# Kernel optimization log

Hardware: AMD Instinct MI355X
Metric: run time of the kernel (lower is better)

Reference implementation:

```python
import jax, jax.numpy as jnp
import numpy as np
from jax import lax

EPS = 1e-5
B, C, H, W = 16, 256, 56, 56
HEADS, DIM_K, DIM_U, DIM_OUT = 4, 16, 4, 256
DIM_V = DIM_OUT // HEADS  # 64
R = 15


def setup_inputs() -> dict:
    key = jax.random.key(0)
    ks = jax.random.split(key, 16)
    s = 0.05
    return {
        "x": jax.random.normal(ks[0], (B, C, H, W), jnp.float32),
        "Wq": jax.random.normal(ks[1], (C, HEADS * DIM_K), jnp.float32) * s,
        "Wk": jax.random.normal(ks[2], (C, DIM_U * DIM_K), jnp.float32) * s,
        "Wv": jax.random.normal(ks[3], (C, DIM_U * DIM_V), jnp.float32) * s,
        "pos_w": jax.random.normal(ks[4], (DIM_K, DIM_U, 1, R, R), jnp.float32) * s,
        "pos_b": jax.random.normal(ks[5], (DIM_K,), jnp.float32) * s,
        "gq": jax.random.uniform(ks[6], (HEADS * DIM_K,), jnp.float32),
        "bq": jax.random.normal(ks[7], (HEADS * DIM_K,), jnp.float32) * s,
        "mq": jax.random.normal(ks[8], (HEADS * DIM_K,), jnp.float32) * s,
        "vq": jax.random.uniform(ks[9], (HEADS * DIM_K,), jnp.float32) + 0.5,
        "gv": jax.random.uniform(ks[10], (DIM_U * DIM_V,), jnp.float32),
        "bv": jax.random.normal(ks[11], (DIM_U * DIM_V,), jnp.float32) * s,
        "mv": jax.random.normal(ks[12], (DIM_U * DIM_V,), jnp.float32) * s,
        "vv": jax.random.uniform(ks[13], (DIM_U * DIM_V,), jnp.float32) + 0.5,
    }


def _bn(x, gamma, beta, mean, var):
    # inference-mode BatchNorm over channel dim (axis=1), x: [b,c,h,w]
    inv = gamma / jnp.sqrt(var + EPS)
    return x * inv[None, :, None, None] + (beta - mean * inv)[None, :, None, None]


def reference(x, Wq, Wk, Wv, pos_w, pos_b, gq, bq, mq, vq, gv, bv, mv, vv):
    b, c, hh, ww = x.shape
    n = hh * ww
    h, dk, u, dv = HEADS, DIM_K, DIM_U, DIM_V
    # 1x1 convs (channels_first) == channel matmuls
    q = jnp.einsum('bchw,cd->bdhw', x, Wq)
    k = jnp.einsum('bchw,cd->bdhw', x, Wk)
    v = jnp.einsum('bchw,cd->bdhw', x, Wv)
    q = _bn(q, gq, bq, mq, vq)
    v = _bn(v, gv, bv, mv, vv)
    # rearranges: 'b (h k) hh ww -> b h k (hh ww)', 'b (u k) hh ww -> b u k n', 'b (u v) hh ww -> b u v n'
    q = q.reshape(b, h, dk, n)
    k = k.reshape(b, u, dk, n)
    v = v.reshape(b, u, dv, n)
    k = jax.nn.softmax(k, axis=-1)  # keras Softmax default axis=-1 (positions)
    # content lambda
    Lc = jnp.einsum('bukm,buvm->bkv', k, v)
    Yc = jnp.einsum('bhkn,bkv->bnhv', q, Lc)
    # position lambda: conv3d over (v,hh,ww) with kernel (1,r,r), pad spatial only
    v5 = v.reshape(b, u, dv, hh, ww)  # [N, C=u, D=v, H, W]
    p = R // 2
    Lp = lax.conv_general_dilated(
        v5, pos_w, window_strides=(1, 1, 1),
        padding=[(0, 0), (p, p), (p, p)],
        dimension_numbers=('NCDHW', 'OIDHW', 'NCDHW'))
    Lp = Lp + pos_b[None, :, None, None, None]  # [b, k, v, hh, ww]
    Lp = Lp.reshape(b, dk, dv, n)
    Yp = jnp.einsum('bhkn,bkvn->bnhv', q, Lp)
    Y = Yc + Yp  # [b, n, h, v]
    # 'b (hh ww) h v -> b (h v) hh ww'
    out = Y.reshape(b, hh, ww, h, dv).transpose(0, 3, 4, 1, 2).reshape(b, h * dv, hh, ww)
    return out
```

## Files before the change

kernel.cpp:

```cpp
#include <hip/hip_runtime.h>
#include <cstdint>
#include <cstddef>

#define NB   16
#define NC   256
#define NPIX 3136
#define NW   56
#define EPSV 1e-5f

#define OFF_AB   0u
#define OFF_BNA  49152u
#define OFF_BNB  49536u
#define OFF_WT   49920u
#define OFF_KS   58112u
#define OFF_LC   59136u
#define OFF_Y    75520u

typedef short bf16x8 __attribute__((ext_vector_type(8)));
typedef float f32x4  __attribute__((ext_vector_type(4)));
typedef float f32x16 __attribute__((ext_vector_type(16)));

__device__ __forceinline__ uint32_t f2bf(float f) {
  uint32_t x = __float_as_uint(f);
  uint32_t r = x + 0x7fffu + ((x >> 16) & 1u);
  return r >> 16;
}
__device__ __forceinline__ uint32_t pk_trunc(float a, float b) {
  return (__float_as_uint(a) >> 16) | (__float_as_uint(b) & 0xffff0000u);
}

__device__ __forceinline__ float fetchW(const float* Wq, const float* Wk,
                                        const float* Wv, int m, int c) {
  if (m < 64)  return Wq[c * 64 + m];
  if (m < 128) return Wk[c * 64 + (m - 64)];
  return Wv[c * 256 + (m - 128)];
}

__global__ void prep_kernel(const float* __restrict__ Wq, const float* __restrict__ Wk,
                            const float* __restrict__ Wv, const float* __restrict__ pos_w,
                            const float* __restrict__ gq, const float* __restrict__ bq,
                            const float* __restrict__ mq, const float* __restrict__ vq,
                            const float* __restrict__ gv, const float* __restrict__ bv,
                            const float* __restrict__ mv, const float* __restrict__ vv,
                            float* __restrict__ ws) {
  int d = blockIdx.x;
  int c = threadIdx.x;
  int i = d * 256 + c;
  if (i < 49152) {
    int dgt = i >> 12, rem = i & 4095;
    int kc = rem >> 8, rem2 = rem & 255;
    int lane = rem2 >> 2, dp = rem2 & 3;
    int m = dgt * 32 + (lane & 31);
    int k0 = kc * 16 + (lane >> 5) * 8 + dp * 2;
    float w0 = fetchW(Wq, Wk, Wv, m, k0);
    float w1 = fetchW(Wq, Wk, Wv, m, k0 + 1);
    ((uint32_t*)(ws + OFF_AB))[i] = f2bf(w0) | (f2bf(w1) << 16);
  }
  if (c == 0) {
    float sa, sb;
    if (d < 64)        { float inv = gq[d] / sqrtf(vq[d] + EPSV); sa = inv; sb = bq[d] - mq[d] * inv; }
    else if (d < 128)  { sa = 1.0f; sb = 0.0f; }
    else               { int j = d - 128; float inv = gv[j] / sqrtf(vv[j] + EPSV); sa = inv; sb = bv[j] - mv[j] * inv; }
    ws[OFF_BNA + d] = sa;
    ws[OFF_BNB + d] = sb;
  }
  if (i < 8192) {
    int chunk = i >> 8, rem = i & 255, lane = rem >> 2, dp = rem & 3;
    int quad = lane >> 4, k = lane & 15;
    int u = chunk >> 3, t = chunk & 7;
    int dh = 2 * t + (quad >> 1);
    int dwb = (quad & 1) * 8 + dp * 2;
    float w0 = (dh < 15 && dwb     < 15) ? pos_w[k * 900 + u * 225 + dh * 15 + dwb]     : 0.0f;
    float w1 = (dh < 15 && dwb + 1 < 15) ? pos_w[k * 900 + u * 225 + dh * 15 + dwb + 1] : 0.0f;
    ((uint32_t*)(ws + OFF_WT))[i] = f2bf(w0) | (f2bf(w1) << 16);
  }
  if (i < 1024) ws[OFF_KS + i] = 0.0f;
}

__launch_bounds__(256, 2)
__global__ void qkv_mfma(const float* __restrict__ x, const float* __restrict__ wsc,
                         float* __restrict__ Y) {
  __shared__ uint32_t X[64 * 128];
  __shared__ float BNs[768];
  int tid = threadIdx.x;
  int n0 = blockIdx.x * 64, b = blockIdx.y;
  for (int i = tid; i < 768; i += 256) BNs[i] = wsc[OFF_BNA + i];
  const size_t xb = (size_t)b * NC * NPIX;
#pragma unroll
  for (int it = 0; it < 4; ++it) {
    int n2 = tid & 31;
    int cp4 = it * 8 + (tid >> 5);
    const float* xp = x + xb + (size_t)(cp4 * 8) * NPIX + n0 + n2 * 2;
    float2 ld[8];
#pragma unroll
    for (int j = 0; j < 8; ++j) ld[j] = *(const float2*)(xp + (size_t)j * NPIX);
    uint32_t e0, e1, e2, e3, o0, o1, o2, o3;
    e0 = f2bf(ld[0].x) | (f2bf(ld[1].x) << 16);
    e1 = f2bf(ld[2].x) | (f2bf(ld[3].x) << 16);
    e2 = f2bf(ld[4].x) | (f2bf(ld[5].x) << 16);
    e3 = f2bf(ld[6].x) | (f2bf(ld[7].x) << 16);
    o0 = f2bf(ld[0].y) | (f2bf(ld[1].y) << 16);
    o1 = f2bf(ld[2].y) | (f2bf(ld[3].y) << 16);
    o2 = f2bf(ld[4].y) | (f2bf(ld[5].y) << 16);
    o3 = f2bf(ld[6].y) | (f2bf(ld[7].y) << 16);
    int ne = 2 * n2, no = ne + 1;
    uint4 ve; ve.x = e0; ve.y = e1; ve.z = e2; ve.w = e3;
    uint4 vo; vo.x = o0; vo.y = o1; vo.z = o2; vo.w = o3;
    *(uint4*)(X + ne * 128 + ((cp4 ^ (ne & 31)) << 2)) = ve;
    *(uint4*)(X + no * 128 + ((cp4 ^ (no & 31)) << 2)) = vo;
  }
  __syncthreads();
  int lane = tid & 63, w = tid >> 6;
  int n31 = lane & 31, h5 = lane >> 5;
  f32x16 acc[3][2];
#pragma unroll
  for (int dt = 0; dt < 3; ++dt)
#pragma unroll
    for (int nt = 0; nt < 2; ++nt)
#pragma unroll
      for (int e = 0; e < 16; ++e) acc[dt][nt][e] = 0.0f;
  const uint4* AB = (const uint4*)(wsc + OFF_AB);
#pragma unroll 4
  for (int kc = 0; kc < 16; ++kc) {
    bf16x8 af[3];
#pragma unroll
    for (int dt = 0; dt < 3; ++dt) {
      union { uint4 q; bf16x8 v; } tmp;
      tmp.q = AB[(size_t)(((w * 3 + dt) * 16 + kc)) * 64 + lane];
      af[dt] = tmp.v;
    }
#pragma unroll
    for (int nt = 0; nt < 2; ++nt) {
      union { uint4 q; bf16x8 v; } bu;
      bu.q = *(const uint4*)(X + (nt * 32 + n31) * 128 + (((2 * kc + h5) ^ n31) << 2));
#pragma unroll
      for (int dt = 0; dt < 3; ++dt)
        acc[dt][nt] = __builtin_amdgcn_mfma_f32_32x32x16_bf16(af[dt], bu.v, acc[dt][nt], 0, 0, 0);
    }
  }
#pragma unroll
  for (int dt = 0; dt < 3; ++dt) {
    int dgt = w * 3 + dt;
    float sa[16], sb[16];
#pragma unroll
    for (int g = 0; g < 4; ++g) {
      *(float4*)(sa + g * 4) = *(const float4*)(BNs + dgt * 32 + g * 8 + h5 * 4);
      *(float4*)(sb + g * 4) = *(const float4*)(BNs + 384 + dgt * 32 + g * 8 + h5 * 4);
    }
#pragma unroll
    for (int nt = 0; nt < 2; ++nt) {
      int pix = n0 + nt * 32 + n31;
      if (dgt < 2) {
        uint2* qb2 = (uint2*)(Y + (size_t)b * 384 * NPIX);
#pragma unroll
        for (int g = 0; g < 4; ++g) {
          float y0 = fmaf(acc[dt][nt][4 * g + 0], sa[4 * g + 0], sb[4 * g + 0]);
          float y1 = fmaf(acc[dt][nt][4 * g + 1], sa[4 * g + 1], sb[4 * g + 1]);
          float y2 = fmaf(acc[dt][nt][4 * g + 2], sa[4 * g + 2], sb[4 * g + 2]);
          float y3 = fmaf(acc[dt][nt][4 * g + 3], sa[4 * g + 3], sb[4 * g + 3]);
          uint2 val;
          val.x = f2bf(y0) | (f2bf(y1) << 16);
          val.y = f2bf(y2) | (f2bf(y3) << 16);
          qb2[(size_t)(dgt * 8 + 2 * g + h5) * NPIX + pix] = val;
        }
      } else {
#pragma unroll
        for (int g = 0; g < 4; ++g)
#pragma unroll
          for (int ki = 0; ki < 4; ++ki) {
            int d = dgt * 32 + 8 * g + 4 * h5 + ki;
            Y[((size_t)b * 384 + d) * NPIX + pix] =
                fmaf(acc[dt][nt][4 * g + ki], sa[4 * g + ki], sb[4 * g + ki]);
          }
      }
    }
  }
}

__launch_bounds__(256)
__global__ void lc_mfma(float* __restrict__ Y, float* __restrict__ ws) {
  __shared__ float R[4096];
  __shared__ float Rs[64];
  int bx = blockIdx.x, u = blockIdx.y, b = blockIdx.z;
  int tid = threadIdx.x;
  int lane = tid & 63, w = tid >> 6;
  int col = lane & 15, quad = lane >> 4;
  int slot = bx * 4 + w;
  const float* krow  = Y + ((size_t)(b * 384 + 64 + u * 16 + col)) * NPIX;
  const float* vbase = Y + ((size_t)(b * 384 + 128 + u * 64 + col)) * NPIX;
  f32x4 acc[4];
#pragma unroll
  for (int vt = 0; vt < 4; ++vt) acc[vt] = (f32x4){0.f, 0.f, 0.f, 0.f};
  float ssum = 0.0f;
  for (int c = slot; c < 98; c += 64) {
    int n0 = c * 32 + quad * 8;
    float4 k0 = *(const float4*)(krow + n0);
    float4 k1 = *(const float4*)(krow + n0 + 4);
    float e0 = __expf(k0.x), e1 = __expf(k0.y), e2 = __expf(k0.z), e3 = __expf(k0.w);
    float e4 = __expf(k1.x), e5 = __expf(k1.y), e6 = __expf(k1.z), e7 = __expf(k1.w);
    ssum += (e0 + e1 + e2 + e3) + (e4 + e5 + e6 + e7);
    union { uint32_t d[4]; bf16x8 v; } kb;
    kb.d[0] = pk_trunc(e0, e1);
    kb.d[1] = pk_trunc(e2, e3);
    kb.d[2] = pk_trunc(e4, e5);
    kb.d[3] = pk_trunc(e6, e7);
#pragma unroll
    for (int vt = 0; vt < 4; ++vt) {
      const float* vp = vbase + (size_t)(vt * 16) * NPIX + n0;
      float4 v0 = *(const float4*)(vp);
      float4 v1 = *(const float4*)(vp + 4);
      union { uint32_t d[4]; bf16x8 v; } vb;
      vb.d[0] = pk_trunc(v0.x, v0.y);
      vb.d[1] = pk_trunc(v0.z, v0.w);
      vb.d[2] = pk_trunc(v1.x, v1.y);
      vb.d[3] = pk_trunc(v1.z, v1.w);
      acc[vt] = __builtin_amdgcn_mfma_f32_16x16x32_bf16(vb.v, kb.v, acc[vt], 0, 0, 0);
    }
  }
  ssum += __shfl_xor(ssum, 16);
  ssum += __shfl_xor(ssum, 32);
#pragma unroll
  for (int vt = 0; vt < 4; ++vt)
#pragma unroll
    for (int r = 0; r < 4; ++r)
      R[w * 1024 + vt * 256 + quad * 64 + r * 16 + col] = acc[vt][r];
  if (lane < 16) Rs[w * 16 + col] = ssum;
  __syncthreads();
  float* P = Y + (size_t)b * 384 * NPIX + 32 * NPIX + (size_t)(u * 16 + bx) * 1024;
  float4 s0 = *(const float4*)(R + tid * 4);
  float4 s1 = *(const float4*)(R + 1024 + tid * 4);
  float4 s2 = *(const float4*)(R + 2048 + tid * 4);
  float4 s3 = *(const float4*)(R + 3072 + tid * 4);
  float4 tot;
  tot.x = (s0.x + s1.x) + (s2.x + s3.x);
  tot.y = (s0.y + s1.y) + (s2.y + s3.y);
  tot.z = (s0.z + s1.z) + (s2.z + s3.z);
  tot.w = (s0.w + s1.w) + (s2.w + s3.w);
  *(float4*)(P + tid * 4) = tot;
  if (tid < 16)
    atomicAdd(&ws[OFF_KS + b * 64 + u * 16 + tid],
              (Rs[tid] + Rs[16 + tid]) + (Rs[32 + tid] + Rs[48 + tid]));
}

__global__ void lc_reduce(const float* __restrict__ Y, float* __restrict__ ws) {
  int i = blockIdx.x, b = blockIdx.y;
  int t = threadIdx.x;
  __shared__ float invS[64];
  if (t < 64) invS[t] = 1.0f / ws[OFF_KS + b * 64 + t];
  __syncthreads();
  int idx = i * 256 + t;
  int k = idx & 15, v = idx >> 4;
  const float* P = Y + (size_t)b * 384 * NPIX + 32 * NPIX;
  float tot = 0.0f;
#pragma unroll
  for (int u = 0; u < 4; ++u) {
    float su = 0.0f;
#pragma unroll
    for (int s = 0; s < 16; ++s) su += P[(size_t)(u * 16 + s) * 1024 + idx];
    tot += su * invS[u * 16 + k];
  }
  ws[OFF_LC + (b * 16 + k) * 64 + v] = tot;
}

#define ROWS   29
#define RSTR2  74
#define UPITCH2 2146
#define LDSW2  8584

__launch_bounds__(512, 4)
__global__ void pos_lambda_mfma(const float* __restrict__ Y, const float* __restrict__ wsc,
                                const float* __restrict__ pos_b, float* __restrict__ out) {
  __shared__ uint32_t S[LDSW2];
  int v = blockIdx.x, b = blockIdx.y, band = blockIdx.z;
  int rb = band * 14;
  int tid = threadIdx.x;
  const float* vplane = Y + ((size_t)(b * 384 + 128)) * NPIX + v * NPIX;
  for (int ii = tid; ii < 4292; ii += 512) {
    int u = ii / 1073;
    int rem = ii - u * 1073;
    int row = rem / 37;
    int pr = rem - row * 37;
    int gr = rb + row - 7;
    int grc = min(max(gr, 0), NW - 1);
    bool rv = (gr >= 0) && (gr < NW);
    const float* vp = vplane + (size_t)(u * 64) * NPIX + grc * NW;
    int g0 = 2 * pr - 7;
    float e[3];
#pragma unroll
    for (int j = 0; j < 3; ++j) {
      int g = g0 + j;
      int gc = min(max(g, 0), NW - 1);
      float val = vp[gc];
      e[j] = (rv && g >= 0 && g < NW) ? val : 0.0f;
    }
    uint2 dd;
    dd.x = pk_trunc(e[0], e[1]);
    dd.y = pk_trunc(e[1], e[2]);
    *(uint2*)(S + u * UPITCH2 + row * RSTR2 + 2 * pr) = dd;
  }
  __syncthreads();
  int lane = tid & 63, wid = tid >> 6;
  int quad = lane >> 4, n = lane & 15;
  int dhp = quad >> 1;
  int ct = wid & 3, p = wid >> 2;
  int cb = (ct == 3) ? 40 : ct * 16;
  int sb = cb + n + (quad & 1) * 8;
  int abase = (p + dhp) * RSTR2 + sb;
  const uint4* wt = (const uint4*)(wsc + OFF_WT);
  f32x4 acc[7];
#pragma unroll
  for (int q = 0; q < 7; ++q) acc[q] = (f32x4){0.f, 0.f, 0.f, 0.f};
#pragma unroll 1
  for (int u = 0; u < 4; ++u) {
    bf16x8 wf[8];
#pragma unroll
    for (int t = 0; t < 8; ++t) {
      union { uint4 q; bf16x8 v; } tmp;
      tmp.q = wt[(u * 8 + t) * 64 + lane];
      wf[t] = tmp.v;
    }
    int au = u * UPITCH2 + abase;
#pragma unroll
    for (int PP = 0; PP < 14; ++PP) {
      int a = au + PP * (2 * RSTR2);
      union { uint32_t u4[4]; bf16x8 v8; } bu;
      bu.u4[0] = S[a];     bu.u4[1] = S[a + 2];
      bu.u4[2] = S[a + 4]; bu.u4[3] = S[a + 6];
#pragma unroll
      for (int t = 0; t < 8; ++t) {
        int q = PP - t;
        if (q >= 0 && q < 7)
          acc[q] = __builtin_amdgcn_mfma_f32_16x16x32_bf16(wf[t], bu.v8, acc[q], 0, 0, 0);
      }
    }
  }
  float lcq[4];
#pragma unroll
  for (int r = 0; r < 4; ++r) {
    int k = quad * 4 + r;
    lcq[r] = wsc[OFF_LC + (b * 16 + k) * 64 + v] + pos_b[k];
  }
  const uint2* qb2 = (const uint2*)(Y + (size_t)b * 384 * NPIX);
#pragma unroll
  for (int q = 0; q < 7; ++q) {
    int rr = rb + p + 2 * q;
    int pix = rr * NW + cb + n;
    float m0 = acc[q][0] + lcq[0], m1 = acc[q][1] + lcq[1];
    float m2 = acc[q][2] + lcq[2], m3 = acc[q][3] + lcq[3];
    float pp[4];
#pragma unroll
    for (int j = 0; j < 4; ++j) {
      int h = quad ^ j;
      uint2 qd = qb2[(h * 4 + quad) * NPIX + pix];
      float q0 = __uint_as_float(qd.x << 16);
      float q1 = __uint_as_float(qd.x & 0xffff0000u);
      float q2 = __uint_as_float(qd.y << 16);
      float q3 = __uint_as_float(qd.y & 0xffff0000u);
      pp[j] = fmaf(q0, m0, fmaf(q1, m1, fmaf(q2, m2, q3 * m3)));
    }
    float t0 = pp[0] + __shfl_xor(pp[1], 16);
    float t2 = pp[2] + __shfl_xor(pp[3], 16);
    float y  = t0 + __shfl_xor(t2, 32);
    out[((size_t)(b * 256 + quad * 64 + v)) * NPIX + pix] = y;
  }
}

extern "C" void kernel_launch(void* const* d_in, const int* in_sizes, int n_in,
                              void* d_out, int out_size, void* d_ws, size_t ws_size,
                              hipStream_t stream) {
  const float* x     = (const float*)d_in[0];
  const float* Wq    = (const float*)d_in[1];
  const float* Wk    = (const float*)d_in[2];
  const float* Wv    = (const float*)d_in[3];
  const float* pos_w = (const float*)d_in[4];
  const float* pos_b = (const float*)d_in[5];
  const float* gq    = (const float*)d_in[6];
  const float* bq    = (const float*)d_in[7];
  const float* mq    = (const float*)d_in[8];
  const float* vq    = (const float*)d_in[9];
  const float* gv    = (const float*)d_in[10];
  const float* bv    = (const float*)d_in[11];
  const float* mv    = (const float*)d_in[12];
  const float* vv    = (const float*)d_in[13];
  float* ws  = (float*)d_ws;
  float* out = (float*)d_out;
  float* Y   = ws + OFF_Y;

  prep_kernel<<<dim3(384), 256, 0, stream>>>(Wq, Wk, Wv, pos_w, gq, bq, mq, vq,
                                             gv, bv, mv, vv, ws);
  qkv_mfma<<<dim3(49, 16), 256, 0, stream>>>(x, ws, Y);
  lc_mfma<<<dim3(16, 4, 16), 256, 0, stream>>>(Y, ws);
  lc_reduce<<<dim3(4, 16), 256, 0, stream>>>(Y, ws);
  pos_lambda_mfma<<<dim3(64, 16, 4), 512, 0, stream>>>(Y, ws, pos_b, out);
}
```

Measured before the change: 267.1 us.

## Store V as zero-padded bf16 planes to simplify position-lambda staging

The QKV kernel now writes the V projection as bf16 into row-padded planes (72-wide rows with 8-column zero halos), which an init pass zeros once. The content-lambda kernel reads V directly as packed bf16 and masks pad columns of K with a large negative value. The position-lambda kernel builds its shifted LDS tiles from aligned dword loads with alignbit instead of per-element fp32 loads and bounds checks. It also seeds its accumulators with the content lambda plus bias. Together these halve V traffic and cut address arithmetic, at the cost of extra zero-fill writes and extra padded pixels in the lc loop.

```diff
diff --git a/kernel.cpp b/kernel.cpp
--- a/kernel.cpp
+++ b/kernel.cpp
@@ -7,6 +7,11 @@
 #define NPIX 3136
 #define NW   56
 #define EPSV 1e-5f
+
+#define BSTR   (384 * NPIX)
+#define OFF_VP (128 * NPIX)
+#define VROWD  36
+#define VPLANE (56 * VROWD)
 
 #define OFF_AB   0u
 #define OFF_BNA  49152u
@@ -75,6 +80,15 @@
     ((uint32_t*)(ws + OFF_WT))[i] = f2bf(w0) | (f2bf(w1) << 16);
   }
   if (i < 1024) ws[OFF_KS + i] = 0.0f;
+  for (int g = i; g < 4096 * 56; g += 98304) {
+    int plane = g / 56, r = g - plane * 56;
+    int bb = plane >> 8, d2 = plane & 255;
+    uint32_t* row = (uint32_t*)(ws + OFF_Y) + (size_t)bb * BSTR + OFF_VP
+                    + (size_t)d2 * VPLANE + r * VROWD;
+    uint4 z; z.x = 0; z.y = 0; z.z = 0; z.w = 0;
+    *(uint4*)(row)      = z;
+    *(uint4*)(row + 32) = z;
+  }
 }
 
 __launch_bounds__(256, 2)
@@ -151,7 +165,7 @@
     for (int nt = 0; nt < 2; ++nt) {
       int pix = n0 + nt * 32 + n31;
       if (dgt < 2) {
-        uint2* qb2 = (uint2*)(Y + (size_t)b * 384 * NPIX);
+        uint2* qb2 = (uint2*)(Y + (size_t)b * BSTR);
 #pragma unroll
         for (int g = 0; g < 4; ++g) {
           float y0 = fmaf(acc[dt][nt][4 * g + 0], sa[4 * g + 0], sb[4 * g + 0]);
@@ -163,7 +177,7 @@
           val.y = f2bf(y2) | (f2bf(y3) << 16);
           qb2[(size_t)(dgt * 8 + 2 * g + h5) * NPIX + pix] = val;
         }
-      } else {
+      } else if (dgt < 4) {
 #pragma unroll
         for (int g = 0; g < 4; ++g)
 #pragma unroll
@@ -171,6 +185,18 @@
             int d = dgt * 32 + 8 * g + 4 * h5 + ki;
             Y[((size_t)b * 384 + d) * NPIX + pix] =
                 fmaf(acc[dt][nt][4 * g + ki], sa[4 * g + ki], sb[4 * g + ki]);
+          }
+      } else {
+        int pr = pix / NW, pc = pix - pr * NW;
+        int ridx = pr * 72 + 8 + pc;
+        unsigned short* vp = (unsigned short*)(Y + (size_t)b * BSTR + OFF_VP);
+#pragma unroll
+        for (int g = 0; g < 4; ++g)
+#pragma unroll
+          for (int ki = 0; ki < 4; ++ki) {
+            int d2 = dgt * 32 + 8 * g + 4 * h5 + ki - 128;
+            float yv = fmaf(acc[dt][nt][4 * g + ki], sa[4 * g + ki], sb[4 * g + ki]);
+            vp[(size_t)d2 * 4032 + ridx] = (unsigned short)f2bf(yv);
           }
       }
     }
@@ -186,16 +212,27 @@
   int lane = tid & 63, w = tid >> 6;
   int col = lane & 15, quad = lane >> 4;
   int slot = bx * 4 + w;
-  const float* krow  = Y + ((size_t)(b * 384 + 64 + u * 16 + col)) * NPIX;
-  const float* vbase = Y + ((size_t)(b * 384 + 128 + u * 64 + col)) * NPIX;
+  const float* krow = Y + ((size_t)(b * 384 + 64 + u * 16 + col)) * NPIX;
+  const uint32_t* vpb = (const uint32_t*)(Y + (size_t)b * BSTR + OFF_VP)
+                        + (size_t)(u * 64 + col) * VPLANE;
   f32x4 acc[4];
 #pragma unroll
   for (int vt = 0; vt < 4; ++vt) acc[vt] = (f32x4){0.f, 0.f, 0.f, 0.f};
   float ssum = 0.0f;
-  for (int c = slot; c < 98; c += 64) {
-    int n0 = c * 32 + quad * 8;
-    float4 k0 = *(const float4*)(krow + n0);
-    float4 k1 = *(const float4*)(krow + n0 + 4);
+  for (int c = slot; c < 126; c += 64) {
+    int p0 = c * 32 + quad * 8;
+    int row = p0 / 72;
+    int pc = p0 - row * 72;
+    bool valid = (unsigned)(pc - 8) < 56u;
+    float4 k0, k1;
+    if (valid) {
+      const float* kp = krow + row * NW + pc - 8;
+      k0 = *(const float4*)(kp);
+      k1 = *(const float4*)(kp + 4);
+    } else {
+      k0.x = k0.y = k0.z = k0.w = -1e30f;
+      k1 = k0;
+    }
     float e0 = __expf(k0.x), e1 = __expf(k0.y), e2 = __expf(k0.z), e3 = __expf(k0.w);
     float e4 = __expf(k1.x), e5 = __expf(k1.y), e6 = __expf(k1.z), e7 = __expf(k1.w);
     ssum += (e0 + e1 + e2 + e3) + (e4 + e5 + e6 + e7);
@@ -204,16 +241,11 @@
     kb.d[1] = pk_trunc(e2, e3);
     kb.d[2] = pk_trunc(e4, e5);
     kb.d[3] = pk_trunc(e6, e7);
+    int vdw = c * 16 + quad * 4;
 #pragma unroll
     for (int vt = 0; vt < 4; ++vt) {
-      const float* vp = vbase + (size_t)(vt * 16) * NPIX + n0;
-      float4 v0 = *(const float4*)(vp);
-      float4 v1 = *(const float4*)(vp + 4);
-      union { uint32_t d[4]; bf16x8 v; } vb;
-      vb.d[0] = pk_trunc(v0.x, v0.y);
-      vb.d[1] = pk_trunc(v0.z, v0.w);
-      vb.d[2] = pk_trunc(v1.x, v1.y);
-      vb.d[3] = pk_trunc(v1.z, v1.w);
+      union { uint4 q; bf16x8 v; } vb;
+      vb.q = *(const uint4*)(vpb + (size_t)(vt * 16) * VPLANE + vdw);
       acc[vt] = __builtin_amdgcn_mfma_f32_16x16x32_bf16(vb.v, kb.v, acc[vt], 0, 0, 0);
     }
   }
@@ -226,7 +258,7 @@
       R[w * 1024 + vt * 256 + quad * 64 + r * 16 + col] = acc[vt][r];
   if (lane < 16) Rs[w * 16 + col] = ssum;
   __syncthreads();
-  float* P = Y + (size_t)b * 384 * NPIX + 32 * NPIX + (size_t)(u * 16 + bx) * 1024;
+  float* P = Y + (size_t)b * BSTR + 32 * NPIX + (size_t)(u * 16 + bx) * 1024;
   float4 s0 = *(const float4*)(R + tid * 4);
   float4 s1 = *(const float4*)(R + 1024 + tid * 4);
   float4 s2 = *(const float4*)(R + 2048 + tid * 4);
@@ -249,8 +281,8 @@
   if (t < 64) invS[t] = 1.0f / ws[OFF_KS + b * 64 + t];
   __syncthreads();
   int idx = i * 256 + t;
-  int k = idx & 15, v = idx >> 4;
-  const float* P = Y + (size_t)b * 384 * NPIX + 32 * NPIX;
+  int k = idx & 15;
+  const float* P = Y + (size_t)b * BSTR + 32 * NPIX;
   float tot = 0.0f;
 #pragma unroll
   for (int u = 0; u < 4; ++u) {
@@ -259,44 +291,41 @@
     for (int s = 0; s < 16; ++s) su += P[(size_t)(u * 16 + s) * 1024 + idx];
     tot += su * invS[u * 16 + k];
   }
-  ws[OFF_LC + (b * 16 + k) * 64 + v] = tot;
-}
-
-#define ROWS   29
-#define RSTR2  74
-#define UPITCH2 2146
-#define LDSW2  8584
+  ws[OFF_LC + (b * 16 + k) * 64 + (idx >> 4)] = tot;
+}
+
+#define ROWS    29
+#define RSTR2   72
+#define UPITCH2 2088
+#define LDSW2   8352
 
 __launch_bounds__(512, 4)
 __global__ void pos_lambda_mfma(const float* __restrict__ Y, const float* __restrict__ wsc,
                                 const float* __restrict__ pos_b, float* __restrict__ out) {
-  __shared__ uint32_t S[LDSW2];
+  __shared__ __attribute__((aligned(16))) uint32_t S[LDSW2];
   int v = blockIdx.x, b = blockIdx.y, band = blockIdx.z;
   int rb = band * 14;
   int tid = threadIdx.x;
-  const float* vplane = Y + ((size_t)(b * 384 + 128)) * NPIX + v * NPIX;
-  for (int ii = tid; ii < 4292; ii += 512) {
-    int u = ii / 1073;
-    int rem = ii - u * 1073;
-    int row = rem / 37;
-    int pr = rem - row * 37;
+  const uint32_t* vpad = (const uint32_t*)(Y + (size_t)b * BSTR + OFF_VP);
+  for (int ii = tid; ii < 1044; ii += 512) {
+    int u = ii / 261;
+    int rem = ii - u * 261;
+    int row = rem / 9;
+    int j3 = rem - row * 9;
     int gr = rb + row - 7;
-    int grc = min(max(gr, 0), NW - 1);
-    bool rv = (gr >= 0) && (gr < NW);
-    const float* vp = vplane + (size_t)(u * 64) * NPIX + grc * NW;
-    int g0 = 2 * pr - 7;
-    float e[3];
-#pragma unroll
-    for (int j = 0; j < 3; ++j) {
-      int g = g0 + j;
-      int gc = min(max(g, 0), NW - 1);
-      float val = vp[gc];
-      e[j] = (rv && g >= 0 && g < NW) ? val : 0.0f;
-    }
-    uint2 dd;
-    dd.x = pk_trunc(e[0], e[1]);
-    dd.y = pk_trunc(e[1], e[2]);
-    *(uint2*)(S + u * UPITCH2 + row * RSTR2 + 2 * pr) = dd;
+    uint32_t d0 = 0, d1 = 0, d2 = 0, d3 = 0, d4 = 0;
+    if ((unsigned)gr < (unsigned)NW) {
+      const uint32_t* pr32 = vpad + (size_t)(u * 64 + v) * VPLANE + gr * VROWD + 4 * j3;
+      d0 = pr32[0]; d1 = pr32[1]; d2 = pr32[2]; d3 = pr32[3]; d4 = pr32[4];
+    }
+    uint32_t* dst = S + u * UPITCH2 + row * RSTR2 + 8 * j3;
+    uint4 w0, w1;
+    w0.x = __builtin_amdgcn_alignbit(d1, d0, 16);  w0.y = d1;
+    w0.z = __builtin_amdgcn_alignbit(d2, d1, 16);  w0.w = d2;
+    w1.x = __builtin_amdgcn_alignbit(d3, d2, 16);  w1.y = d3;
+    w1.z = __builtin_amdgcn_alignbit(d4, d3, 16);  w1.w = d4;
+    *(uint4*)(dst)     = w0;
+    *(uint4*)(dst + 4) = w1;
   }
   __syncthreads();
   int lane = tid & 63, wid = tid >> 6;
@@ -307,9 +336,17 @@
   int sb = cb + n + (quad & 1) * 8;
   int abase = (p + dhp) * RSTR2 + sb;
   const uint4* wt = (const uint4*)(wsc + OFF_WT);
+  float lcq[4];
+#pragma unroll
+  for (int r = 0; r < 4; ++r) {
+    int k = quad * 4 + r;
+    lcq[r] = wsc[OFF_LC + (b * 16 + k) * 64 + v] + pos_b[k];
+  }
   f32x4 acc[7];
 #pragma unroll
-  for (int q = 0; q < 7; ++q) acc[q] = (f32x4){0.f, 0.f, 0.f, 0.f};
+  for (int q = 0; q < 7; ++q) {
+    acc[q][0] = lcq[0]; acc[q][1] = lcq[1]; acc[q][2] = lcq[2]; acc[q][3] = lcq[3];
+  }
 #pragma unroll 1
   for (int u = 0; u < 4; ++u) {
     bf16x8 wf[8];
@@ -334,19 +371,13 @@
       }
     }
   }
-  float lcq[4];
-#pragma unroll
-  for (int r = 0; r < 4; ++r) {
-    int k = quad * 4 + r;
-    lcq[r] = wsc[OFF_LC + (b * 16 + k) * 64 + v] + pos_b[k];
-  }
-  const uint2* qb2 = (const uint2*)(Y + (size_t)b * 384 * NPIX);
+  const uint2* qb2 = (const uint2*)(Y + (size_t)b * BSTR);
 #pragma unroll
   for (int q = 0; q < 7; ++q) {
     int rr = rb + p + 2 * q;
     int pix = rr * NW + cb + n;
-    float m0 = acc[q][0] + lcq[0], m1 = acc[q][1] + lcq[1];
-    float m2 = acc[q][2] + lcq[2], m3 = acc[q][3] + lcq[3];
+    float m0 = acc[q][0], m1 = acc[q][1];
+    float m2 = acc[q][2], m3 = acc[q][3];
     float pp[4];
 #pragma unroll
     for (int j = 0; j < 4; ++j) {
```

Result: faster. 261.1 us (-2.3%).
